# Optimization experiments

Measured on AMD Instinct MI355X. Metric: run time of the kernel, lower is better.

Reference implementation:

```python
import jax, jax.numpy as jnp
import numpy as np

MASK_SUB = 1000000.0  # the module subtracts 1e6 from masked scores (not -inf)

def setup_inputs() -> dict:
    key = jax.random.key(0)
    kq, kk, kv = jax.random.split(key, 3)
    B, S, D = 16, 2048, 64
    q = jax.random.normal(kq, (B, S, D), dtype=jnp.float32)
    k = jax.random.normal(kk, (B, S, D), dtype=jnp.float32)
    v = jax.random.normal(kv, (B, S, D), dtype=jnp.float32)
    return {"q": q, "k": k, "v": v}

def reference(q, k, v):
    d_k = k.shape[-1]
    s = k.shape[-2]
    # scores: [b, s_q, s_k]
    scores = jnp.einsum('bqd,bkd->bqk', q, k) / jnp.sqrt(jnp.asarray(d_k, q.dtype))
    # causal mask: strictly-upper-triangular entries get 1e6 subtracted (matches torch.triu diagonal=1)
    causal = jnp.triu(jnp.ones((s, s), dtype=bool), k=1)
    scores = jnp.where(causal[None, :, :], scores - MASK_SUB, scores)
    weights = jax.nn.softmax(scores, axis=-1)
    return jnp.einsum('bqk,bkd->bqd', weights, v)
```

## Files before the change

### kernel.cpp

```cpp
#include <hip/hip_runtime.h>
#include <stdint.h>


typedef __bf16 bf16x8 __attribute__((ext_vector_type(8)));
typedef float f32x4 __attribute__((ext_vector_type(4)));
typedef float f32x16 __attribute__((ext_vector_type(16)));
typedef uint32_t u32x4 __attribute__((ext_vector_type(4)));

#define NB 16
#define SL 2048
#define DH 64

__device__ __forceinline__ __bf16 f2bf(float f) {
    uint32_t u = __builtin_bit_cast(uint32_t, f);
    u += 0x7FFFu + ((u >> 16) & 1u);
    uint16_t h = (uint16_t)(u >> 16);
    return __builtin_bit_cast(__bf16, h);
}

__device__ __forceinline__ uint32_t cvtpk(float lo, float hi) {
    uint32_t r;
    asm("v_cvt_pk_bf16_f32 %0, %1, %2" : "=v"(r) : "v"(lo), "v"(hi));
    return r;
}

__device__ __forceinline__ void load_lds16(const void* g, void* l) {
    __builtin_amdgcn_global_load_lds(
        (const __attribute__((address_space(1))) uint32_t*)g,
        (__attribute__((address_space(3))) uint32_t*)l, 16, 0, 0);
}

__global__ __launch_bounds__(256) void prepass(
        const float* __restrict__ K, const float* __restrict__ V,
        __bf16* __restrict__ Kb, __bf16* __restrict__ Vt) {
    __shared__ float tl[64][68];
    const int b    = blockIdx.x >> 5;
    const int tile = blockIdx.x & 31;
    const int s0   = tile << 6;
    const int t    = threadIdx.x;
    const int r    = t >> 2;
    const int c0   = (t & 3) * 16;

    const float* Kp = K + ((size_t)(b * SL + s0) + r) * DH + c0;
    float4 f0 = ((const float4*)Kp)[0], f1 = ((const float4*)Kp)[1];
    float4 f2 = ((const float4*)Kp)[2], f3 = ((const float4*)Kp)[3];
    bf16x8 w0, w1;
    w0[0]=f2bf(f0.x); w0[1]=f2bf(f0.y); w0[2]=f2bf(f0.z); w0[3]=f2bf(f0.w);
    w0[4]=f2bf(f1.x); w0[5]=f2bf(f1.y); w0[6]=f2bf(f1.z); w0[7]=f2bf(f1.w);
    w1[0]=f2bf(f2.x); w1[1]=f2bf(f2.y); w1[2]=f2bf(f2.z); w1[3]=f2bf(f2.w);
    w1[4]=f2bf(f3.x); w1[5]=f2bf(f3.y); w1[6]=f2bf(f3.z); w1[7]=f2bf(f3.w);
    __bf16* Kbp = Kb + ((size_t)(b * SL + s0) + r) * DH;
    const int j0 = c0 >> 3;
    *(bf16x8*)(Kbp + ((j0       ^ (r & 7)) * 8)) = w0;
    *(bf16x8*)(Kbp + (((j0 + 1) ^ (r & 7)) * 8)) = w1;

    const float* Vp = V + ((size_t)(b * SL + s0) + r) * DH + c0;
    ((float4*)&tl[r][c0])[0] = ((const float4*)Vp)[0];
    ((float4*)&tl[r][c0])[1] = ((const float4*)Vp)[1];
    ((float4*)&tl[r][c0])[2] = ((const float4*)Vp)[2];
    ((float4*)&tl[r][c0])[3] = ((const float4*)Vp)[3];
    __syncthreads();

    __bf16* img = Vt + ((size_t)(b * 32 + tile)) * 4096;
#pragma unroll
    for (int half = 0; half < 2; ++half) {
        const int c = half * 256 + t;
        const int d = c >> 3, slot = c & 7;
        const int jj = slot ^ (d & 7);
        bf16x8 w;
#pragma unroll
        for (int e = 0; e < 8; ++e) w[e] = f2bf(tl[jj * 8 + e][d]);
        *(bf16x8*)(img + c * 8) = w;
    }
}

__global__ __launch_bounds__(256, 4) void attn_fwd(
        const float* __restrict__ Q, const __bf16* __restrict__ Kb,
        const __bf16* __restrict__ Vt, float* __restrict__ part,
        float* __restrict__ lpart) {
    __shared__ __align__(16) __bf16 lK[2][4096];
    __shared__ __align__(16) __bf16 lV[2][4096];

    const int bid = blockIdx.x;
    const int b   = bid & 15;
    const int j   = 39 - (bid >> 4);
    int qb, c;
    if (j < 4)        { qb = j;                 c = 0; }
    else if (j < 12)  { qb = 4 + ((j - 4) >> 1);  c = (j - 4) & 1; }
    else if (j < 24)  { int k = j - 12; qb = 8 + k / 3;    c = k % 3; }
    else              { int k = j - 24; qb = 12 + (k >> 2); c = k & 3; }
    const int nt  = 2 * qb + 2;
    const int kt0 = c * 8;
    const int kt1 = min(kt0 + 8, nt);

    const int tid  = threadIdx.x;
    const int wave = tid >> 6, lane = tid & 63;
    const int h    = lane >> 5, l32 = lane & 31, x8 = lane & 7;
    const int qg   = qb * 128 + wave * 32 + l32;
    const int dt   = 2 * qb + (wave >> 1);

    const float QSC = 0.125f * 1.44269504088896340736f;
    bf16x8 qf[4];
    const float* qp = Q + ((size_t)b * SL + qg) * DH + h * 8;
#pragma unroll
    for (int s4 = 0; s4 < 4; ++s4) {
        float4 a0 = ((const float4*)(qp + s4 * 16))[0];
        float4 a1 = ((const float4*)(qp + s4 * 16))[1];
        qf[s4][0] = f2bf(a0.x * QSC); qf[s4][1] = f2bf(a0.y * QSC);
        qf[s4][2] = f2bf(a0.z * QSC); qf[s4][3] = f2bf(a0.w * QSC);
        qf[s4][4] = f2bf(a1.x * QSC); qf[s4][5] = f2bf(a1.y * QSC);
        qf[s4][6] = f2bf(a1.z * QSC); qf[s4][7] = f2bf(a1.w * QSC);
    }

    f32x16 acc0 = (f32x16)0.0f, acc1 = (f32x16)0.0f;
    float lsa0 = 0.f, lsa1 = 0.f, lsa2 = 0.f, lsa3 = 0.f;

    const __bf16* Kbase = Kb + (size_t)b * SL * DH;
    const __bf16* Vbase = Vt + (size_t)b * 32 * 4096;

    auto stage = [&](int kt2) {
        const int bufi = kt2 & 1;
        const __bf16* Ks = Kbase + (size_t)kt2 * 4096;
        const __bf16* Vs = Vbase + (size_t)kt2 * 4096;
#pragma unroll
        for (int i2 = 0; i2 < 2; ++i2) {
            load_lds16(Ks + (size_t)(i2 * 256 + tid) * 8,
                       &lK[bufi][(i2 * 256 + wave * 64) * 8]);
            load_lds16(Vs + (size_t)(i2 * 256 + tid) * 8,
                       &lV[bufi][(i2 * 256 + wave * 64) * 8]);
        }
    };

    __builtin_amdgcn_sched_barrier(0);
    stage(kt0);
    stage(kt0 + 1);

    for (int kt = kt0; kt < kt1; ++kt) {
        if (kt + 1 < kt1) asm volatile("s_waitcnt vmcnt(4)" ::: "memory");
        else              asm volatile("s_waitcnt vmcnt(0)" ::: "memory");
        asm volatile("s_barrier" ::: "memory");
        const __bf16* K_ = lK[kt & 1];
        const __bf16* V_ = lV[kt & 1];

        const bool skip = (wave < 2) && (kt == nt - 1);
        if (!skip) {
            f32x16 sc0 = (f32x16)0.0f, sc1 = (f32x16)0.0f;
            __builtin_amdgcn_s_setprio(1);
#pragma unroll
            for (int s4 = 0; s4 < 4; ++s4) {
                bf16x8 kf0 = *(const bf16x8*)&K_[(l32)      * 64 + (((s4 * 2 + h) ^ x8) << 3)];
                bf16x8 kf1 = *(const bf16x8*)&K_[(32 + l32) * 64 + (((s4 * 2 + h) ^ x8) << 3)];
                sc0 = __builtin_amdgcn_mfma_f32_32x32x16_bf16(kf0, qf[s4], sc0, 0, 0, 0);
                sc1 = __builtin_amdgcn_mfma_f32_32x32x16_bf16(kf1, qf[s4], sc1, 0, 0, 0);
            }
            __builtin_amdgcn_s_setprio(0);

            if (kt >= dt) {
                const int kb = kt * 64;
#pragma unroll
                for (int r = 0; r < 16; ++r) {
                    const int krow = (r & 3) + 8 * (r >> 2) + 4 * h;
                    if (kb + krow > qg)      sc0[r] = -1.0e30f;
                    if (kb + 32 + krow > qg) sc1[r] = -1.0e30f;
                }
            }

#pragma unroll
            for (int r = 0; r < 16; ++r) {
                sc0[r] = __builtin_amdgcn_exp2f(sc0[r]);
                sc1[r] = __builtin_amdgcn_exp2f(sc1[r]);
            }
#pragma unroll
            for (int r = 0; r < 16; r += 4) {
                lsa0 += sc0[r + 0] + sc1[r + 0];
                lsa1 += sc0[r + 1] + sc1[r + 1];
                lsa2 += sc0[r + 2] + sc1[r + 2];
                lsa3 += sc0[r + 3] + sc1[r + 3];
            }

            bf16x8 af[4];
#pragma unroll
            for (int ks = 0; ks < 4; ++ks) {
                const int jj = (ks & 1) * 8;
                const f32x16& sg = (ks & 2) ? sc1 : sc0;
                uint32_t u0 = cvtpk(sg[jj + 0], sg[jj + 1]);
                uint32_t u1 = cvtpk(sg[jj + 2], sg[jj + 3]);
                uint32_t u2 = cvtpk(sg[jj + 4], sg[jj + 5]);
                uint32_t u3 = cvtpk(sg[jj + 6], sg[jj + 7]);
                auto r0 = __builtin_amdgcn_permlane32_swap(u0, u2, false, false);
                auto r1 = __builtin_amdgcn_permlane32_swap(u1, u3, false, false);
                u32x4 w; w[0] = r0[0]; w[1] = r1[0]; w[2] = r0[1]; w[3] = r1[1];
                af[ks] = __builtin_bit_cast(bf16x8, w);
            }

            __builtin_amdgcn_s_setprio(1);
#pragma unroll
            for (int ks = 0; ks < 4; ++ks) {
                bf16x8 vf0 = *(const bf16x8*)&V_[(l32)      * 64 + ((((ks << 1) + h) ^ x8) << 3)];
                bf16x8 vf1 = *(const bf16x8*)&V_[(32 + l32) * 64 + ((((ks << 1) + h) ^ x8) << 3)];
                acc0 = __builtin_amdgcn_mfma_f32_32x32x16_bf16(af[ks], vf0, acc0, 0, 0, 0);
                acc1 = __builtin_amdgcn_mfma_f32_32x32x16_bf16(af[ks], vf1, acc1, 0, 0, 0);
            }
            __builtin_amdgcn_s_setprio(0);
        }

        asm volatile("s_barrier" ::: "memory");
        if (kt + 2 < kt1) stage(kt + 2);
    }

    float ls = (lsa0 + lsa1) + (lsa2 + lsa3);
    ls += __shfl_xor(ls, 32);

#pragma unroll
    for (int r = 0; r < 16; ++r) {
        const int qrow = qb * 128 + wave * 32 + (r & 3) + 8 * (r >> 2) + 4 * h;
        float* pp = part + ((size_t)(b * SL + qrow) * 4 + c) * DH + l32;
        pp[0]  = acc0[r];
        pp[32] = acc1[r];
    }
    if (h == 0)
        lpart[(size_t)(b * SL + qg) * 4 + c] = ls;
}

__global__ __launch_bounds__(256) void combine(
        const float* __restrict__ part, const float* __restrict__ lpart,
        float* __restrict__ O) {
    const int tid = threadIdx.x;
    const int r   = blockIdx.x * 16 + (tid >> 4);
    const int d4  = tid & 15;
    const int qb  = (r >> 7) & 15;
    const int nch = (2 * qb + 9) >> 3;
    float4 s = make_float4(0.f, 0.f, 0.f, 0.f);
    float ls = 0.f;
    for (int c = 0; c < nch; ++c) {
        float4 p = *(const float4*)(part + ((size_t)r * 4 + c) * DH + d4 * 4);
        s.x += p.x; s.y += p.y; s.z += p.z; s.w += p.w;
        ls += lpart[(size_t)r * 4 + c];
    }
    const float inv = 1.0f / ls;
    float4 o; o.x = s.x * inv; o.y = s.y * inv; o.z = s.z * inv; o.w = s.w * inv;
    *(float4*)(O + (size_t)r * DH + d4 * 4) = o;
}

extern "C" void kernel_launch(void* const* d_in, const int* in_sizes, int n_in,
                              void* d_out, int out_size, void* d_ws, size_t ws_size,
                              hipStream_t stream) {
    const float* q = (const float*)d_in[0];
    const float* k = (const float*)d_in[1];
    const float* v = (const float*)d_in[2];
    float* o = (float*)d_out;
    __bf16* Kb   = (__bf16*)d_ws;
    __bf16* Vt   = Kb + (size_t)NB * SL * DH;
    float*  pt   = (float*)((char*)d_ws + (8u << 20));
    float*  lp   = pt + (size_t)NB * SL * 4 * DH;
    hipLaunchKernelGGL(prepass, dim3(NB * 32), dim3(256), 0, stream, k, v, Kb, Vt);
    hipLaunchKernelGGL(attn_fwd, dim3(640), dim3(256), 0, stream, q, Kb, Vt, pt, lp);
    hipLaunchKernelGGL(combine, dim3(NB * SL / 16), dim3(256), 0, stream, pt, lp, o);
}
```

Baseline: 97.20 us.

## Fuse split-K combine into attention kernel via atomic tickets

Removes the separate combine launch. Query blocks that need only one key chunk now normalise and write the output directly. For split blocks, the last chunk to finish (found by an atomic ticket counter reset in the prepass) reduces the partials. This cuts one kernel launch and the partial-buffer round trip for single-chunk rows, at the cost of extra barriers, atomics and a serialized tail reduction inside the attention blocks.

```diff
diff --git a/kernel.cpp b/kernel.cpp
--- a/kernel.cpp
+++ b/kernel.cpp
@@ -32,12 +32,15 @@
 
 __global__ __launch_bounds__(256) void prepass(
         const float* __restrict__ K, const float* __restrict__ V,
-        __bf16* __restrict__ Kb, __bf16* __restrict__ Vt) {
+        __bf16* __restrict__ Kb, __bf16* __restrict__ Vt,
+        int* __restrict__ tickets) {
     __shared__ float tl[64][68];
+    const int t = threadIdx.x;
+    if (blockIdx.x == 0) tickets[t] = 0;
+
     const int b    = blockIdx.x >> 5;
     const int tile = blockIdx.x & 31;
     const int s0   = tile << 6;
-    const int t    = threadIdx.x;
     const int r    = t >> 2;
     const int c0   = (t & 3) * 16;
 
@@ -77,9 +80,12 @@
 __global__ __launch_bounds__(256, 4) void attn_fwd(
         const float* __restrict__ Q, const __bf16* __restrict__ Kb,
         const __bf16* __restrict__ Vt, float* __restrict__ part,
-        float* __restrict__ lpart) {
+        float* __restrict__ lpart, int* __restrict__ tickets,
+        float* __restrict__ O) {
     __shared__ __align__(16) __bf16 lK[2][4096];
     __shared__ __align__(16) __bf16 lV[2][4096];
+    __shared__ float lsw[128];
+    __shared__ int winflag;
 
     const int bid = blockIdx.x;
     const int b   = bid & 15;
@@ -90,6 +96,7 @@
     else if (j < 24)  { int k = j - 12; qb = 8 + k / 3;    c = k % 3; }
     else              { int k = j - 24; qb = 12 + (k >> 2); c = k & 3; }
     const int nt  = 2 * qb + 2;
+    const int nch = (2 * qb + 9) >> 3;
     const int kt0 = c * 8;
     const int kt1 = min(kt0 + 8, nt);
 
@@ -210,6 +217,20 @@
 
     float ls = (lsa0 + lsa1) + (lsa2 + lsa3);
     ls += __shfl_xor(ls, 32);
+    if (h == 0) lsw[wave * 32 + l32] = ls;
+    __syncthreads();
+
+    if (nch == 1) {
+        float* Ob = O + ((size_t)(b * SL + qb * 128 + wave * 32)) * DH;
+#pragma unroll
+        for (int r = 0; r < 16; ++r) {
+            const int crow = (r & 3) + 8 * (r >> 2) + 4 * h;
+            const float inv = 1.0f / lsw[wave * 32 + crow];
+            Ob[(size_t)crow * DH + l32]      = acc0[r] * inv;
+            Ob[(size_t)crow * DH + l32 + 32] = acc1[r] * inv;
+        }
+        return;
+    }
 
 #pragma unroll
     for (int r = 0; r < 16; ++r) {
@@ -220,26 +241,33 @@
     }
     if (h == 0)
         lpart[(size_t)(b * SL + qg) * 4 + c] = ls;
-}
-
-__global__ __launch_bounds__(256) void combine(
-        const float* __restrict__ part, const float* __restrict__ lpart,
-        float* __restrict__ O) {
-    const int tid = threadIdx.x;
-    const int r   = blockIdx.x * 16 + (tid >> 4);
-    const int d4  = tid & 15;
-    const int qb  = (r >> 7) & 15;
-    const int nch = (2 * qb + 9) >> 3;
-    float4 s = make_float4(0.f, 0.f, 0.f, 0.f);
-    float ls = 0.f;
-    for (int c = 0; c < nch; ++c) {
-        float4 p = *(const float4*)(part + ((size_t)r * 4 + c) * DH + d4 * 4);
-        s.x += p.x; s.y += p.y; s.z += p.z; s.w += p.w;
-        ls += lpart[(size_t)r * 4 + c];
-    }
-    const float inv = 1.0f / ls;
-    float4 o; o.x = s.x * inv; o.y = s.y * inv; o.z = s.z * inv; o.w = s.w * inv;
-    *(float4*)(O + (size_t)r * DH + d4 * 4) = o;
+
+    __syncthreads();
+    if (tid == 0) {
+        const int old = __hip_atomic_fetch_add(&tickets[b * 16 + qb], 1,
+                                               __ATOMIC_ACQ_REL,
+                                               __HIP_MEMORY_SCOPE_AGENT);
+        winflag = (old == nch - 1);
+    }
+    __syncthreads();
+    if (!winflag) return;
+
+    const int row16 = tid >> 4, d4 = tid & 15;
+#pragma unroll
+    for (int i = 0; i < 8; ++i) {
+        const int row = row16 + 16 * i;
+        const size_t gr = (size_t)(b * SL + qb * 128 + row);
+        float4 s = make_float4(0.f, 0.f, 0.f, 0.f);
+        float lsr = 0.f;
+        for (int cc = 0; cc < nch; ++cc) {
+            float4 p = *(const float4*)(part + (gr * 4 + cc) * DH + d4 * 4);
+            s.x += p.x; s.y += p.y; s.z += p.z; s.w += p.w;
+            lsr += lpart[gr * 4 + cc];
+        }
+        const float inv = 1.0f / lsr;
+        float4 o; o.x = s.x * inv; o.y = s.y * inv; o.z = s.z * inv; o.w = s.w * inv;
+        *(float4*)(O + gr * DH + d4 * 4) = o;
+    }
 }
 
 extern "C" void kernel_launch(void* const* d_in, const int* in_sizes, int n_in,
@@ -253,7 +281,7 @@
     __bf16* Vt   = Kb + (size_t)NB * SL * DH;
     float*  pt   = (float*)((char*)d_ws + (8u << 20));
     float*  lp   = pt + (size_t)NB * SL * 4 * DH;
-    hipLaunchKernelGGL(prepass, dim3(NB * 32), dim3(256), 0, stream, k, v, Kb, Vt);
-    hipLaunchKernelGGL(attn_fwd, dim3(640), dim3(256), 0, stream, q, Kb, Vt, pt, lp);
-    hipLaunchKernelGGL(combine, dim3(NB * SL / 16), dim3(256), 0, stream, pt, lp, o);
-}
+    int*    tk   = (int*)(lp + (size_t)NB * SL * 4);
+    hipLaunchKernelGGL(prepass, dim3(NB * 32), dim3(256), 0, stream, k, v, Kb, Vt, tk);
+    hipLaunchKernelGGL(attn_fwd, dim3(640), dim3(256), 0, stream, q, Kb, Vt, pt, lp, tk, o);
+}
```

Result: slower. 117.9 us (+21.3%).
